# Optimization experiments

Hardware: AMD Instinct MI355X
Metric: run time of the kernel (lower is better)

The kernel has to match this reference:

```python
import jax, jax.numpy as jnp
import numpy as np

NUM_EMBEDDINGS = 16384
EMBEDDING_DIM = 256
B, C, H, W = 8, 256, 32, 32


def _l2_normalize(x, axis=-1, eps=1e-12):
    # matches torch.nn.functional.normalize(p=2): x / max(||x||, eps)
    n = jnp.sqrt(jnp.sum(x * x, axis=axis, keepdims=True))
    return x / jnp.maximum(n, eps)


def setup_inputs() -> dict:
    key = jax.random.key(0)
    k1, k2 = jax.random.split(key)
    z = jax.random.normal(k1, (B, C, H, W), dtype=jnp.float32)
    embedding_weight = jax.random.normal(k2, (NUM_EMBEDDINGS, EMBEDDING_DIM), dtype=jnp.float32)
    return {"z": z, "embedding_weight": embedding_weight}


def reference(z, embedding_weight):
    batch_size, channels, height, width = z.shape
    # [B,C,H,W] -> [B,H,W,C] -> [N, D]
    z_flat = jnp.transpose(z, (0, 2, 3, 1)).reshape(-1, EMBEDDING_DIM)
    z_flat = _l2_normalize(z_flat)                 # l2_norm=True
    emb = _l2_normalize(embedding_weight)
    # squared distances: ||z||^2 + ||e||^2 - 2 z e^T  -> [N, K]
    d = (jnp.sum(z_flat * z_flat, axis=1, keepdims=True)
         + jnp.sum(emb * emb, axis=1)
         - 2.0 * jnp.matmul(z_flat, emb.T))
    indices = jnp.argmin(d, axis=1)                # [N]
    z_q = emb[indices].reshape(batch_size, height, width, EMBEDDING_DIM)
    z_q = jnp.transpose(z_q, (0, 3, 1, 2))         # [B,C,H,W]
    indices = indices.reshape(batch_size, height, width)
    return z_q, indices
```

## Files before the change

### kernel.cpp

```cpp
#include <hip/hip_runtime.h>

#define NUM_E   16384
#define DIM     256
#define NROWS   8192
#define HW      1024
#define BM      128
#define BN      256
#define BK      32
#define NCB     (NUM_E / BN)
#define GATE    2e-3f
#define TAUC    2e-3f
#define EHID    2e-3
#define MAXC    16

#define SWZ(r) ((((r) >> 1) ^ ((r) >> 3)) & 3)

typedef __bf16 bf16x8 __attribute__((ext_vector_type(8)));
typedef float  f32x4  __attribute__((ext_vector_type(4)));
typedef float  f32x16 __attribute__((ext_vector_type(16)));

__device__ __forceinline__ unsigned short f2bf(float x) {
    unsigned u = __float_as_uint(x);
    unsigned r = (u + 0x7fffu + ((u >> 16) & 1u)) >> 16;
    return (unsigned short)r;
}
__device__ __forceinline__ void async_copy16(const void* g, void* l) {
    __builtin_amdgcn_global_load_lds(
        (const __attribute__((address_space(1))) unsigned int*)g,
        (__attribute__((address_space(3))) unsigned int*)l, 16, 0, 0);
}

__global__ void k_sumz(const float* __restrict__ z, float* __restrict__ zpart) {
    int n = blockIdx.x * 256 + threadIdx.x;
    int b = n >> 10, hw = n & 1023;
    int cb = blockIdx.y;
    const float* p = z + (size_t)(b * DIM + cb * 16) * HW + hw;
    float s = 0.f;
    #pragma unroll
    for (int c = 0; c < 16; c++) { float v = p[c * HW]; s += v * v; }
    zpart[cb * NROWS + n] = s;
}

__global__ void k_prep_z(const float* __restrict__ z, const float* __restrict__ zpart,
                         unsigned short* __restrict__ Zh) {
    __shared__ float T[64 * 68];
    __shared__ __align__(16) float Tinv[64];
    int t = threadIdx.x;
    int n0 = blockIdx.x * 64, c0 = blockIdx.y * 64;
    int b = n0 >> 10, hw0 = n0 & 1023;
    if (t < 64) {
        float s = 0.f;
        #pragma unroll
        for (int cb = 0; cb < 16; cb++) s += zpart[cb * NROWS + n0 + t];
        Tinv[t] = 1.0f / fmaxf(sqrtf(s), 1e-12f);
    }
    __syncthreads();
    #pragma unroll
    for (int i = 0; i < 4; i++) {
        int f = t + 256 * i;
        int cc = f >> 4, n4 = (f & 15) * 4;
        float4 v  = *(const float4*)(z + (size_t)(b * DIM + c0 + cc) * HW + hw0 + n4);
        float4 iv = *(const float4*)&Tinv[n4];
        v.x *= iv.x; v.y *= iv.y; v.z *= iv.z; v.w *= iv.w;
        *(float4*)&T[cc * 68 + n4] = v;
    }
    __syncthreads();
    #pragma unroll
    for (int i = 0; i < 4; i++) {
        int f = t + 256 * i;
        int nn = f >> 4, c4 = (f & 15) * 4;
        ushort4 h;
        h.x = f2bf(T[(c4+0)*68 + nn]);
        h.y = f2bf(T[(c4+1)*68 + nn]);
        h.z = f2bf(T[(c4+2)*68 + nn]);
        h.w = f2bf(T[(c4+3)*68 + nn]);
        *(ushort4*)(Zh + (size_t)(n0 + nn) * DIM + c0 + c4) = h;
    }
}

__global__ void k_prep_e(const float* __restrict__ emb, float* __restrict__ inv_e,
                         double* __restrict__ se2, unsigned short* __restrict__ Eh,
                         int* __restrict__ cnt, int* __restrict__ cnt2) {
    if (blockIdx.x == 0 && threadIdx.x == 0) { *cnt = 0; *cnt2 = 0; }
    int wv = threadIdx.x >> 6, lane = threadIdx.x & 63;
    int k = blockIdx.x * 4 + wv;
    float4 v = *(const float4*)(emb + (size_t)k * DIM + lane * 4);
    double sq = (double)v.x*v.x + (double)v.y*v.y + (double)v.z*v.z + (double)v.w*v.w;
    for (int off = 32; off > 0; off >>= 1) sq += __shfl_down(sq, off);
    double tot = fmax(__shfl(sq, 0), 1e-24);
    if (lane == 0) { se2[k] = tot; inv_e[k] = 1.0f / fmaxf((float)sqrt(tot), 1e-12f); }
    float s = 1.0f / fmaxf((float)sqrt(tot), 1e-12f);
    ushort4 h;
    h.x = f2bf(v.x * s); h.y = f2bf(v.y * s); h.z = f2bf(v.z * s); h.w = f2bf(v.w * s);
    *(ushort4*)(Eh + (size_t)k * DIM + lane * 4) = h;
}

__launch_bounds__(256, 2)
__global__ void k_score(const unsigned short* __restrict__ Zh,
                        const unsigned short* __restrict__ Eh, f32x4* __restrict__ part) {
    __shared__ __align__(16) float smem[16896];
    unsigned short* lds = (unsigned short*)smem;
    float* vals = smem;
    int*   idxs = (int*)(smem + 8448);
    const int t = threadIdx.x, l = t & 63, w = t >> 6;
    const int wm = w >> 1, wn = w & 1;
    const int m0 = blockIdx.x * BM;
    const int nb = blockIdx.y * BN;
    const int l31 = l & 31, lh = l >> 5;
    const int sr = l >> 2, sp = l & 3;

    const unsigned short* gA0 = Zh + (size_t)m0 * DIM;
    const unsigned short* gB0 = Eh + (size_t)nb * DIM;

    f32x16 acc[2][4];
    #pragma unroll
    for (int i = 0; i < 2; i++)
        #pragma unroll
        for (int j = 0; j < 4; j++) acc[i][j] = (f32x16)0.f;

    for (int kc = 0; kc < DIM; kc += BK) {
        {
            #pragma unroll
            for (int h = 0; h < 2; h++) {
                int sub = 4 * h + w;
                int r = sub * 16 + sr;
                int c = sp ^ SWZ(r);
                async_copy16(gA0 + (size_t)r * DIM + kc + c * 8, &lds[sub * 512]);
            }
        }
        #pragma unroll
        for (int h = 0; h < 4; h++) {
            int sub = 4 * h + w;
            int r = sub * 16 + sr;
            int c = sp ^ SWZ(r);
            async_copy16(gB0 + (size_t)r * DIM + kc + c * 8, &lds[4096 + sub * 512]);
        }
        __syncthreads();
        #pragma unroll
        for (int s = 0; s < 2; s++) {
            int c = 2 * s + lh;
            bf16x8 ah[2], bh[4];
            #pragma unroll
            for (int i = 0; i < 2; i++) {
                int r = wm * 64 + i * 32 + l31;
                ah[i] = *(const bf16x8*)&lds[r * 32 + ((c ^ SWZ(r)) * 8)];
            }
            #pragma unroll
            for (int j = 0; j < 4; j++) {
                int r = wn * 128 + j * 32 + l31;
                bh[j] = *(const bf16x8*)&lds[4096 + r * 32 + ((c ^ SWZ(r)) * 8)];
            }
            #pragma unroll
            for (int i = 0; i < 2; i++)
                #pragma unroll
                for (int j = 0; j < 4; j++)
                    acc[i][j] = __builtin_amdgcn_mfma_f32_32x32x16_bf16(ah[i], bh[j], acc[i][j], 0, 0, 0);
        }
        __syncthreads();
    }

    float VA1 = -2e9f, VA2 = -2e9f, VB1 = -2e9f, VB2 = -2e9f;
    int JA1 = 0, JA2 = 0, JB1 = 0, JB2 = 0;
    const int rl = t >> 2, q = t & 3;
    #pragma unroll
    for (int i = 0; i < 2; i++) {
        #pragma unroll
        for (int reg = 0; reg < 16; reg++) {
            float V1 = -2e9f, V2 = -2e9f; int I1 = 0, I2 = 0;
            #pragma unroll
            for (int j = 0; j < 4; j++) {
                float v = acc[i][j][reg];
                int c = nb + wn * 128 + j * 32 + l31;
                bool g1 = v > V1, g2 = v > V2;
                I2 = g1 ? I1 : (g2 ? c : I2);
                V2 = g1 ? V1 : (g2 ? v : V2);
                I1 = g1 ? c : I1;
                V1 = g1 ? v : V1;
            }
            int rr = wm * 32 + (reg & 3) + 8 * (reg >> 2) + 4 * lh;
            int s0 = wn * 64 + l31 * 2;
            int a0 = rr * 132 + (s0 >> 5) * 33 + (s0 & 31);
            vals[a0] = V1; vals[a0 + 1] = V2;
            idxs[a0] = I1; idxs[a0 + 1] = I2;
        }
        __syncthreads();
        float V1 = -2e9f, V2 = -2e9f; int I1 = 0, I2 = 0;
        const float* pv = &vals[rl * 132 + q * 33];
        const int*   pi = &idxs[rl * 132 + q * 33];
        #pragma unroll
        for (int u = 0; u < 32; u++) {
            float v = pv[u]; int c = pi[u];
            bool g1 = v > V1, g2 = v > V2;
            I2 = g1 ? I1 : (g2 ? c : I2);
            V2 = g1 ? V1 : (g2 ? v : V2);
            I1 = g1 ? c : I1;
            V1 = g1 ? v : V1;
        }
        __syncthreads();
        #pragma unroll
        for (int d = 1; d <= 2; d <<= 1) {
            float oV1 = __shfl_down(V1, d), oV2 = __shfl_down(V2, d);
            int   oI1 = __shfl_down(I1, d), oI2 = __shfl_down(I2, d);
            bool o1 = oV1 > V1;
            float mn = o1 ? V1 : oV1; int mni = o1 ? I1 : oI1;
            V1 = o1 ? oV1 : V1; I1 = o1 ? oI1 : I1;
            bool s2 = oV2 > V2;
            float m2 = s2 ? oV2 : V2; int m2i = s2 ? oI2 : I2;
            bool c2 = m2 > mn;
            V2 = c2 ? m2 : mn; I2 = c2 ? m2i : mni;
        }
        if (i == 0) {
            bool o1 = V1 > VA1;
            float mn = o1 ? VA1 : V1; int mni = o1 ? JA1 : I1;
            VA1 = o1 ? V1 : VA1; JA1 = o1 ? I1 : JA1;
            bool s2 = V2 > VA2;
            float m2 = s2 ? V2 : VA2; int m2i = s2 ? I2 : JA2;
            bool c2 = m2 > mn;
            VA2 = c2 ? m2 : mn; JA2 = c2 ? m2i : mni;
        } else {
            bool o1 = V1 > VB1;
            float mn = o1 ? VB1 : V1; int mni = o1 ? JB1 : I1;
            VB1 = o1 ? V1 : VB1; JB1 = o1 ? I1 : JB1;
            bool s2 = V2 > VB2;
            float m2 = s2 ? V2 : VB2; int m2i = s2 ? I2 : JB2;
            bool c2 = m2 > mn;
            VB2 = c2 ? m2 : mn; JB2 = c2 ? m2i : mni;
        }
    }
    if ((t & 3) == 0) {
        int rowA = (rl >> 5) * 64 + (rl & 31);
        int rowB = rowA + 32;
        f32x4 ea; ea[0] = VA1; ea[1] = __int_as_float(JA1);
        ea[2] = VA2; ea[3] = __int_as_float(JA2);
        part[(size_t)blockIdx.y * NROWS + m0 + rowA] = ea;
        f32x4 eb; eb[0] = VB1; eb[1] = __int_as_float(JB1);
        eb[2] = VB2; eb[3] = __int_as_float(JB2);
        part[(size_t)blockIdx.y * NROWS + m0 + rowB] = eb;
    }
}

__global__ void k_final(const f32x4* __restrict__ part, int* __restrict__ idx_ws,
                        float* __restrict__ out_idx, int* __restrict__ flags,
                        int* __restrict__ cnt, int* __restrict__ cand,
                        int* __restrict__ ccnt, float* __restrict__ v2q) {
    __shared__ f32x4 red[8][32];
    __shared__ float bcV1[32], bcV2[32];
    __shared__ int   lcc[32];
    __shared__ int   lcand[32][MAXC];
    __shared__ float sv2[8][32];
    const int nl = threadIdx.x & 31, sc = threadIdx.x >> 5;
    const int n = blockIdx.x * 32 + nl;
    if (threadIdx.x < 32) lcc[threadIdx.x] = 0;
    float V1 = -2e9f, V2 = -2e9f; int I1 = 0;
    for (int s = sc * 8; s < sc * 8 + 8; s++) {
        f32x4 e = part[(size_t)s * NROWS + n];
        float v1 = e[0]; int i1 = __float_as_int(e[1]); float v2 = e[2];
        V2 = fmaxf(fmaxf(V2, v2), fminf(v1, V1));
        I1 = (v1 > V1) ? i1 : I1;
        V1 = fmaxf(V1, v1);
    }
    f32x4 me; me[0] = V1; me[1] = __int_as_float(I1); me[2] = V2; me[3] = 0.f;
    red[sc][nl] = me;
    __syncthreads();
    if (threadIdx.x < 32) {
        float W1 = -2e9f, W2 = -2e9f; int J1 = 0;
        #pragma unroll
        for (int s2 = 0; s2 < 8; s2++) {
            f32x4 e = red[s2][threadIdx.x];
            float v1 = e[0]; int i1 = __float_as_int(e[1]); float v2 = e[2];
            W2 = fmaxf(fmaxf(W2, v2), fminf(v1, W1));
            J1 = (v1 > W1) ? i1 : J1;
            W1 = fmaxf(W1, v1);
        }
        int nn = blockIdx.x * 32 + threadIdx.x;
        idx_ws[nn] = J1;
        out_idx[nn] = (float)J1;
        bcV1[threadIdx.x] = W1;
        bcV2[threadIdx.x] = W2;
    }
    __syncthreads();
    float thr = bcV1[nl] - TAUC;
    float lv2 = -2e9f;
    for (int s = sc * 8; s < sc * 8 + 8; s++) {
        f32x4 e = part[(size_t)s * NROWS + n];
        if (e[0] >= thr) {
            int pos = atomicAdd(&lcc[nl], 2);
            if (pos < MAXC)     lcand[nl][pos]     = __float_as_int(e[1]);
            if (pos + 1 < MAXC) lcand[nl][pos + 1] = __float_as_int(e[3]);
            lv2 = fmaxf(lv2, e[2]);
        }
    }
    sv2[sc][nl] = lv2;
    __syncthreads();
    if (threadIdx.x < 32) {
        int nn = blockIdx.x * 32 + threadIdx.x;
        float W1 = bcV1[threadIdx.x], W2 = bcV2[threadIdx.x];
        if (W1 - W2 < GATE) {
            float m = -2e9f;
            #pragma unroll
            for (int s2 = 0; s2 < 8; s2++) m = fmaxf(m, sv2[s2][threadIdx.x]);
            int p = atomicAdd(cnt, 1);
            flags[p] = nn;
            ccnt[nn] = lcc[threadIdx.x];
            v2q[nn] = m;
            #pragma unroll
            for (int j = 0; j < MAXC; j++) cand[nn * MAXC + j] = lcand[threadIdx.x][j];
        }
    }
}

__launch_bounds__(256)
__global__ void k_rescan_cand(const int* __restrict__ flags, const int* __restrict__ cnt,
                              const int* __restrict__ cand, const int* __restrict__ ccnt,
                              const float* __restrict__ v2q,
                              const float* __restrict__ z, const float* __restrict__ emb,
                              const double* __restrict__ se2,
                              int* __restrict__ idx_ws, float* __restrict__ out_idx,
                              int* __restrict__ flags2, int* __restrict__ cnt2) {
    __shared__ double zs[DIM];
    __shared__ double wv[4];
    __shared__ int    wi[4];
    const int t = threadIdx.x, l = t & 63, w = t >> 6;
    const int F = *cnt;
    for (int f = blockIdx.x; f < F; f += gridDim.x) {
        int n = flags[f];
        int C = ccnt[n];
        int b = n >> 10, hw = n & 1023;
        __syncthreads();
        zs[t] = (double)z[(size_t)(b * DIM + t) * HW + hw];
        __syncthreads();
        double best = -2e18; int bi = 0x7fffffff;
        if (C <= MAXC) {
            double z0 = zs[l*4], z1 = zs[l*4+1], z2 = zs[l*4+2], z3 = zs[l*4+3];
            for (int cix = w; cix < C; cix += 4) {
                int k = cand[n * MAXC + cix];
                float4 ev = *(const float4*)(emb + (size_t)k * DIM + l * 4);
                double d = z0 * (double)ev.x + z1 * (double)ev.y
                         + z2 * (double)ev.z + z3 * (double)ev.w;
                #pragma unroll
                for (int o = 32; o > 0; o >>= 1) d += __shfl_down(d, o);
                if (l == 0) {
                    double qv = d / sqrt(se2[k]);
                    if (qv > best || (qv == best && k < bi)) { best = qv; bi = k; }
                }
            }
        }
        if (l == 0) { wv[w] = best; wi[w] = bi; }
        __syncthreads();
        if (t == 0) {
            if (C > MAXC) {
                int p = atomicAdd(cnt2, 1); flags2[p] = n;
            } else {
                double B = wv[0]; int BI = wi[0];
                #pragma unroll
                for (int x = 1; x < 4; x++)
                    if (wv[x] > B || (wv[x] == B && wi[x] < BI)) { B = wv[x]; BI = wi[x]; }
                if ((double)v2q[n] >= B - EHID) {
                    int p = atomicAdd(cnt2, 1); flags2[p] = n;
                } else {
                    idx_ws[n] = BI; out_idx[n] = (float)BI;
                }
            }
        }
    }
}

__launch_bounds__(256)
__global__ void k_fullscan_part(const int* __restrict__ flags2, const int* __restrict__ cnt2,
                                const float* __restrict__ z, const float* __restrict__ emb,
                                const double* __restrict__ se2, double2* __restrict__ partial) {
    __shared__ double zs[DIM];
    __shared__ double wv[4];
    __shared__ int    wi[4];
    const int t = threadIdx.x, l = t & 63, w = t >> 6;
    const int W = (*cnt2) * 64;
    for (int item = blockIdx.x; item < W; item += gridDim.x) {
        int f = item >> 6, split = item & 63;
        int n = flags2[f];
        int b = n >> 10, hw = n & 1023;
        __syncthreads();
        zs[t] = (double)z[(size_t)(b * DIM + t) * HW + hw];
        __syncthreads();
        double z0 = zs[l*4], z1 = zs[l*4+1], z2 = zs[l*4+2], z3 = zs[l*4+3];
        double best = -2e18; int bi = 0;
        int kbase = split * 256 + w * 64;
        for (int p = 0; p < 64; p++) {
            int k = kbase + p;
            float4 ev = *(const float4*)(emb + (size_t)k * DIM + l * 4);
            double d = z0 * (double)ev.x + z1 * (double)ev.y
                     + z2 * (double)ev.z + z3 * (double)ev.w;
            #pragma unroll
            for (int o = 32; o > 0; o >>= 1) d += __shfl_down(d, o);
            if (l == 0) {
                double qv = d / sqrt(se2[k]);
                if (qv > best) { best = qv; bi = k; }
            }
        }
        if (l == 0) { wv[w] = best; wi[w] = bi; }
        __syncthreads();
        if (t == 0) {
            double B = wv[0]; int BI = wi[0];
            #pragma unroll
            for (int x = 1; x < 4; x++)
                if (wv[x] > B || (wv[x] == B && wi[x] < BI)) { B = wv[x]; BI = wi[x]; }
            partial[item] = make_double2(B, (double)BI);
        }
        __syncthreads();
    }
}

__global__ void k_fullscan_merge(const int* __restrict__ flags2, const int* __restrict__ cnt2,
                                 const double2* __restrict__ partial,
                                 int* __restrict__ idx_ws, float* __restrict__ out_idx) {
    const int F = *cnt2;
    const int l = threadIdx.x & 63, w = threadIdx.x >> 6;
    for (int f = blockIdx.x * 4 + w; f < F; f += gridDim.x * 4) {
        double2 e = partial[(size_t)f * 64 + l];
        double v = e.x; int i = (int)e.y;
        #pragma unroll
        for (int o = 32; o > 0; o >>= 1) {
            double ov = __shfl_down(v, o);
            int    oi = __shfl_down(i, o);
            if (ov > v || (ov == v && oi < i)) { v = ov; i = oi; }
        }
        if (l == 0) { int n = flags2[f]; idx_ws[n] = i; out_idx[n] = (float)i; }
    }
}

__global__ void k_zq(const int* __restrict__ idx_ws, const float* __restrict__ emb,
                     const float* __restrict__ inv_e, float* __restrict__ zq) {
    int t = threadIdx.x;
    int n = blockIdx.x * 256 + t;
    int b = n >> 10, hw = n & 1023;
    int c0 = blockIdx.y * 32;
    int id = idx_ws[n];
    float s = inv_e[id];
    const float* er = emb + (size_t)id * DIM;
    #pragma unroll
    for (int cc = 0; cc < 32; cc += 4) {
        float4 a = *(const float4*)(er + c0 + cc);
        zq[(size_t)(b * DIM + c0 + cc + 0) * HW + hw] = a.x * s;
        zq[(size_t)(b * DIM + c0 + cc + 1) * HW + hw] = a.y * s;
        zq[(size_t)(b * DIM + c0 + cc + 2) * HW + hw] = a.z * s;
        zq[(size_t)(b * DIM + c0 + cc + 3) * HW + hw] = a.w * s;
    }
}

extern "C" void kernel_launch(void* const* d_in, const int* in_sizes, int n_in,
                              void* d_out, int out_size, void* d_ws, size_t ws_size,
                              hipStream_t stream) {
    const float* z   = (const float*)d_in[0];
    const float* emb = (const float*)d_in[1];

    unsigned short* Zh = (unsigned short*)d_ws;
    unsigned short* Eh = Zh + (size_t)NROWS * DIM;
    float*  inv_e = (float*)(Eh + (size_t)NUM_E * DIM);
    float*  zpart = inv_e + NUM_E;
    int*    idx_ws = (int*)(zpart + 16 * NROWS);
    double* se2   = (double*)(idx_ws + NROWS);
    int*    flags = (int*)(se2 + NUM_E);
    int*    flags2 = flags + NROWS;
    int*    cand  = flags2 + NROWS;
    int*    ccnt  = cand + NROWS * MAXC;
    float*  v2q   = (float*)(ccnt + NROWS);
    int*    cnt   = (int*)(v2q + NROWS);
    int*    cnt2  = cnt + 1;

    float* zq      = (float*)d_out;
    float* out_idx = zq + (size_t)NROWS * DIM;
    f32x4*   part    = (f32x4*)zq;
    double2* partial = (double2*)zq;

    k_sumz   <<<dim3(NROWS / 256, 16), 256, 0, stream>>>(z, zpart);
    k_prep_z <<<dim3(NROWS / 64, DIM / 64), 256, 0, stream>>>(z, zpart, Zh);
    k_prep_e <<<NUM_E / 4, 256, 0, stream>>>(emb, inv_e, se2, Eh, cnt, cnt2);
    k_score  <<<dim3(NROWS / BM, NCB), 256, 0, stream>>>(Zh, Eh, part);
    k_final  <<<NROWS / 32, 256, 0, stream>>>(part, idx_ws, out_idx, flags, cnt,
                                              cand, ccnt, v2q);
    k_rescan_cand  <<<1024, 256, 0, stream>>>(flags, cnt, cand, ccnt, v2q, z, emb,
                                              se2, idx_ws, out_idx, flags2, cnt2);
    k_fullscan_part<<<2048, 256, 0, stream>>>(flags2, cnt2, z, emb, se2, partial);
    k_fullscan_merge<<<64, 256, 0, stream>>>(flags2, cnt2, partial, idx_ws, out_idx);
    k_zq     <<<dim3(NROWS / 256, 8), 256, 0, stream>>>(idx_ws, emb, inv_e, zq);
}
```

Before: 204.7 us.

## Fuse z-norm into prep, shuffle-based score epilogue, merge candidate rescan into final

Folds the separate sum-of-squares kernel into k_prep_z, so each block loads a full 64-row by 256-channel tile, computes the norms in LDS and writes normalized bf16. The k_score epilogue now reduces top-2 across lanes with xor shuffles instead of an LDS scatter and re-scan, which shrinks shared memory enough to raise launch bounds to 3 blocks per SM. The candidate rescan is done inside k_final using shared-memory candidate lists, removing one launch and the global cand/ccnt/v2q buffers. The costs are a larger LDS tile in prep_z (about 70KB) with fewer blocks, and serial per-flag rescans within each final block.

```diff
diff --git a/kernel.cpp b/kernel.cpp
--- a/kernel.cpp
+++ b/kernel.cpp
@@ -30,58 +30,51 @@
         (__attribute__((address_space(3))) unsigned int*)l, 16, 0, 0);
 }
 
-__global__ void k_sumz(const float* __restrict__ z, float* __restrict__ zpart) {
-    int n = blockIdx.x * 256 + threadIdx.x;
-    int b = n >> 10, hw = n & 1023;
-    int cb = blockIdx.y;
-    const float* p = z + (size_t)(b * DIM + cb * 16) * HW + hw;
-    float s = 0.f;
+__global__ void k_prep_z(const float* __restrict__ z, unsigned short* __restrict__ Zh) {
+    __shared__ float T[256 * 68];
+    __shared__ float Tinv[64];
+    int t = threadIdx.x;
+    int n0 = blockIdx.x * 64;
+    int b = n0 >> 10, hw0 = n0 & 1023;
     #pragma unroll
-    for (int c = 0; c < 16; c++) { float v = p[c * HW]; s += v * v; }
-    zpart[cb * NROWS + n] = s;
-}
-
-__global__ void k_prep_z(const float* __restrict__ z, const float* __restrict__ zpart,
-                         unsigned short* __restrict__ Zh) {
-    __shared__ float T[64 * 68];
-    __shared__ __align__(16) float Tinv[64];
-    int t = threadIdx.x;
-    int n0 = blockIdx.x * 64, c0 = blockIdx.y * 64;
-    int b = n0 >> 10, hw0 = n0 & 1023;
-    if (t < 64) {
-        float s = 0.f;
-        #pragma unroll
-        for (int cb = 0; cb < 16; cb++) s += zpart[cb * NROWS + n0 + t];
-        Tinv[t] = 1.0f / fmaxf(sqrtf(s), 1e-12f);
-    }
-    __syncthreads();
-    #pragma unroll
-    for (int i = 0; i < 4; i++) {
+    for (int i = 0; i < 16; i++) {
         int f = t + 256 * i;
         int cc = f >> 4, n4 = (f & 15) * 4;
-        float4 v  = *(const float4*)(z + (size_t)(b * DIM + c0 + cc) * HW + hw0 + n4);
-        float4 iv = *(const float4*)&Tinv[n4];
-        v.x *= iv.x; v.y *= iv.y; v.z *= iv.z; v.w *= iv.w;
+        float4 v = *(const float4*)(z + (size_t)(b * DIM + cc) * HW + hw0 + n4);
         *(float4*)&T[cc * 68 + n4] = v;
     }
     __syncthreads();
+    {
+        int rl = t >> 2, q = t & 3;
+        float s = 0.f;
+        #pragma unroll
+        for (int c = q * 64; c < q * 64 + 64; c++) {
+            float v = T[c * 68 + rl];
+            s += v * v;
+        }
+        s += __shfl_down(s, 1);
+        s += __shfl_down(s, 2);
+        if (q == 0) Tinv[rl] = 1.0f / fmaxf(sqrtf(s), 1e-12f);
+    }
+    __syncthreads();
     #pragma unroll
-    for (int i = 0; i < 4; i++) {
+    for (int i = 0; i < 16; i++) {
         int f = t + 256 * i;
-        int nn = f >> 4, c4 = (f & 15) * 4;
+        int nn = f >> 6, c4 = (f & 63) * 4;
+        float iv = Tinv[nn];
         ushort4 h;
-        h.x = f2bf(T[(c4+0)*68 + nn]);
-        h.y = f2bf(T[(c4+1)*68 + nn]);
-        h.z = f2bf(T[(c4+2)*68 + nn]);
-        h.w = f2bf(T[(c4+3)*68 + nn]);
-        *(ushort4*)(Zh + (size_t)(n0 + nn) * DIM + c0 + c4) = h;
+        h.x = f2bf(T[(c4+0)*68 + nn] * iv);
+        h.y = f2bf(T[(c4+1)*68 + nn] * iv);
+        h.z = f2bf(T[(c4+2)*68 + nn] * iv);
+        h.w = f2bf(T[(c4+3)*68 + nn] * iv);
+        *(ushort4*)(Zh + (size_t)(n0 + nn) * DIM + c4) = h;
     }
 }
 
 __global__ void k_prep_e(const float* __restrict__ emb, float* __restrict__ inv_e,
                          double* __restrict__ se2, unsigned short* __restrict__ Eh,
-                         int* __restrict__ cnt, int* __restrict__ cnt2) {
-    if (blockIdx.x == 0 && threadIdx.x == 0) { *cnt = 0; *cnt2 = 0; }
+                         int* __restrict__ cnt2) {
+    if (blockIdx.x == 0 && threadIdx.x == 0) *cnt2 = 0;
     int wv = threadIdx.x >> 6, lane = threadIdx.x & 63;
     int k = blockIdx.x * 4 + wv;
     float4 v = *(const float4*)(emb + (size_t)k * DIM + lane * 4);
@@ -95,13 +88,10 @@
     *(ushort4*)(Eh + (size_t)k * DIM + lane * 4) = h;
 }
 
-__launch_bounds__(256, 2)
+__launch_bounds__(256, 3)
 __global__ void k_score(const unsigned short* __restrict__ Zh,
                         const unsigned short* __restrict__ Eh, f32x4* __restrict__ part) {
-    __shared__ __align__(16) float smem[16896];
-    unsigned short* lds = (unsigned short*)smem;
-    float* vals = smem;
-    int*   idxs = (int*)(smem + 8448);
+    __shared__ __align__(16) unsigned short lds[12288];
     const int t = threadIdx.x, l = t & 63, w = t >> 6;
     const int wm = w >> 1, wn = w & 1;
     const int m0 = blockIdx.x * BM;
@@ -119,14 +109,12 @@
         for (int j = 0; j < 4; j++) acc[i][j] = (f32x16)0.f;
 
     for (int kc = 0; kc < DIM; kc += BK) {
-        {
-            #pragma unroll
-            for (int h = 0; h < 2; h++) {
-                int sub = 4 * h + w;
-                int r = sub * 16 + sr;
-                int c = sp ^ SWZ(r);
-                async_copy16(gA0 + (size_t)r * DIM + kc + c * 8, &lds[sub * 512]);
-            }
+        #pragma unroll
+        for (int h = 0; h < 2; h++) {
+            int sub = 4 * h + w;
+            int r = sub * 16 + sr;
+            int c = sp ^ SWZ(r);
+            async_copy16(gA0 + (size_t)r * DIM + kc + c * 8, &lds[sub * 512]);
         }
         #pragma unroll
         for (int h = 0; h < 4; h++) {
@@ -159,9 +147,7 @@
         __syncthreads();
     }
 
-    float VA1 = -2e9f, VA2 = -2e9f, VB1 = -2e9f, VB2 = -2e9f;
-    int JA1 = 0, JA2 = 0, JB1 = 0, JB2 = 0;
-    const int rl = t >> 2, q = t & 3;
+    f32x4* mrg = (f32x4*)lds;
     #pragma unroll
     for (int i = 0; i < 2; i++) {
         #pragma unroll
@@ -177,80 +163,66 @@
                 I1 = g1 ? c : I1;
                 V1 = g1 ? v : V1;
             }
-            int rr = wm * 32 + (reg & 3) + 8 * (reg >> 2) + 4 * lh;
-            int s0 = wn * 64 + l31 * 2;
-            int a0 = rr * 132 + (s0 >> 5) * 33 + (s0 & 31);
-            vals[a0] = V1; vals[a0 + 1] = V2;
-            idxs[a0] = I1; idxs[a0 + 1] = I2;
-        }
-        __syncthreads();
-        float V1 = -2e9f, V2 = -2e9f; int I1 = 0, I2 = 0;
-        const float* pv = &vals[rl * 132 + q * 33];
-        const int*   pi = &idxs[rl * 132 + q * 33];
-        #pragma unroll
-        for (int u = 0; u < 32; u++) {
-            float v = pv[u]; int c = pi[u];
-            bool g1 = v > V1, g2 = v > V2;
-            I2 = g1 ? I1 : (g2 ? c : I2);
-            V2 = g1 ? V1 : (g2 ? v : V2);
-            I1 = g1 ? c : I1;
-            V1 = g1 ? v : V1;
-        }
-        __syncthreads();
-        #pragma unroll
-        for (int d = 1; d <= 2; d <<= 1) {
-            float oV1 = __shfl_down(V1, d), oV2 = __shfl_down(V2, d);
-            int   oI1 = __shfl_down(I1, d), oI2 = __shfl_down(I2, d);
-            bool o1 = oV1 > V1;
-            float mn = o1 ? V1 : oV1; int mni = o1 ? I1 : oI1;
-            V1 = o1 ? oV1 : V1; I1 = o1 ? oI1 : I1;
-            bool s2 = oV2 > V2;
-            float m2 = s2 ? oV2 : V2; int m2i = s2 ? oI2 : I2;
-            bool c2 = m2 > mn;
-            V2 = c2 ? m2 : mn; I2 = c2 ? m2i : mni;
-        }
-        if (i == 0) {
-            bool o1 = V1 > VA1;
-            float mn = o1 ? VA1 : V1; int mni = o1 ? JA1 : I1;
-            VA1 = o1 ? V1 : VA1; JA1 = o1 ? I1 : JA1;
-            bool s2 = V2 > VA2;
-            float m2 = s2 ? V2 : VA2; int m2i = s2 ? I2 : JA2;
-            bool c2 = m2 > mn;
-            VA2 = c2 ? m2 : mn; JA2 = c2 ? m2i : mni;
-        } else {
-            bool o1 = V1 > VB1;
-            float mn = o1 ? VB1 : V1; int mni = o1 ? JB1 : I1;
-            VB1 = o1 ? V1 : VB1; JB1 = o1 ? I1 : JB1;
-            bool s2 = V2 > VB2;
-            float m2 = s2 ? V2 : VB2; int m2i = s2 ? I2 : JB2;
-            bool c2 = m2 > mn;
-            VB2 = c2 ? m2 : mn; JB2 = c2 ? m2i : mni;
-        }
-    }
-    if ((t & 3) == 0) {
-        int rowA = (rl >> 5) * 64 + (rl & 31);
-        int rowB = rowA + 32;
-        f32x4 ea; ea[0] = VA1; ea[1] = __int_as_float(JA1);
-        ea[2] = VA2; ea[3] = __int_as_float(JA2);
-        part[(size_t)blockIdx.y * NROWS + m0 + rowA] = ea;
-        f32x4 eb; eb[0] = VB1; eb[1] = __int_as_float(JB1);
-        eb[2] = VB2; eb[3] = __int_as_float(JB2);
-        part[(size_t)blockIdx.y * NROWS + m0 + rowB] = eb;
-    }
-}
-
-__global__ void k_final(const f32x4* __restrict__ part, int* __restrict__ idx_ws,
-                        float* __restrict__ out_idx, int* __restrict__ flags,
-                        int* __restrict__ cnt, int* __restrict__ cand,
-                        int* __restrict__ ccnt, float* __restrict__ v2q) {
+            #pragma unroll
+            for (int m = 1; m <= 16; m <<= 1) {
+                float oV1 = __shfl_xor(V1, m), oV2 = __shfl_xor(V2, m);
+                int   oI1 = __shfl_xor(I1, m), oI2 = __shfl_xor(I2, m);
+                bool o1 = oV1 > V1;
+                float mn = o1 ? V1 : oV1; int mni = o1 ? I1 : oI1;
+                V1 = o1 ? oV1 : V1; I1 = o1 ? oI1 : I1;
+                bool s2 = oV2 > V2;
+                float m2 = s2 ? oV2 : V2; int m2i = s2 ? oI2 : I2;
+                bool c2 = m2 > mn;
+                V2 = c2 ? m2 : mn; I2 = c2 ? m2i : mni;
+            }
+            if (l31 == 0) {
+                int row = wm * 64 + i * 32 + (reg & 3) + 8 * (reg >> 2) + 4 * lh;
+                f32x4 e; e[0] = V1; e[1] = __int_as_float(I1);
+                e[2] = V2; e[3] = __int_as_float(I2);
+                mrg[row * 2 + wn] = e;
+            }
+        }
+    }
+    __syncthreads();
+    if (t < BM) {
+        f32x4 a = mrg[t * 2], bq = mrg[t * 2 + 1];
+        float V1 = a[0], V2 = a[2]; int I1 = __float_as_int(a[1]), I2 = __float_as_int(a[3]);
+        float oV1 = bq[0], oV2 = bq[2];
+        int   oI1 = __float_as_int(bq[1]), oI2 = __float_as_int(bq[3]);
+        bool o1 = oV1 > V1;
+        float mn = o1 ? V1 : oV1; int mni = o1 ? I1 : oI1;
+        V1 = o1 ? oV1 : V1; I1 = o1 ? oI1 : I1;
+        bool s2 = oV2 > V2;
+        float m2 = s2 ? oV2 : V2; int m2i = s2 ? oI2 : I2;
+        bool c2 = m2 > mn;
+        V2 = c2 ? m2 : mn; I2 = c2 ? m2i : mni;
+        f32x4 e; e[0] = V1; e[1] = __int_as_float(I1);
+        e[2] = V2; e[3] = __int_as_float(I2);
+        part[(size_t)blockIdx.y * NROWS + m0 + t] = e;
+    }
+}
+
+__global__ void k_final(const f32x4* __restrict__ part,
+                        const float* __restrict__ z, const float* __restrict__ emb,
+                        const double* __restrict__ se2,
+                        int* __restrict__ idx_ws, float* __restrict__ out_idx,
+                        int* __restrict__ flags2, int* __restrict__ cnt2) {
     __shared__ f32x4 red[8][32];
-    __shared__ float bcV1[32], bcV2[32];
+    __shared__ float bcV1[32];
     __shared__ int   lcc[32];
     __shared__ int   lcand[32][MAXC];
     __shared__ float sv2[8][32];
-    const int nl = threadIdx.x & 31, sc = threadIdx.x >> 5;
+    __shared__ float mv2[32];
+    __shared__ int   fl[32];
+    __shared__ int   nf;
+    __shared__ double zs[DIM];
+    __shared__ double wvv[4];
+    __shared__ int    wii[4];
+    const int t = threadIdx.x;
+    const int nl = t & 31, sc = t >> 5;
     const int n = blockIdx.x * 32 + nl;
-    if (threadIdx.x < 32) lcc[threadIdx.x] = 0;
+    if (t < 32) lcc[t] = 0;
+    if (t == 0) nf = 0;
     float V1 = -2e9f, V2 = -2e9f; int I1 = 0;
     for (int s = sc * 8; s < sc * 8 + 8; s++) {
         f32x4 e = part[(size_t)s * NROWS + n];
@@ -262,21 +234,21 @@
     f32x4 me; me[0] = V1; me[1] = __int_as_float(I1); me[2] = V2; me[3] = 0.f;
     red[sc][nl] = me;
     __syncthreads();
-    if (threadIdx.x < 32) {
-        float W1 = -2e9f, W2 = -2e9f; int J1 = 0;
+    float W1 = -2e9f, W2 = -2e9f;
+    if (t < 32) {
+        int J1 = 0;
         #pragma unroll
         for (int s2 = 0; s2 < 8; s2++) {
-            f32x4 e = red[s2][threadIdx.x];
+            f32x4 e = red[s2][t];
             float v1 = e[0]; int i1 = __float_as_int(e[1]); float v2 = e[2];
             W2 = fmaxf(fmaxf(W2, v2), fminf(v1, W1));
             J1 = (v1 > W1) ? i1 : J1;
             W1 = fmaxf(W1, v1);
         }
-        int nn = blockIdx.x * 32 + threadIdx.x;
+        int nn = blockIdx.x * 32 + t;
         idx_ws[nn] = J1;
         out_idx[nn] = (float)J1;
-        bcV1[threadIdx.x] = W1;
-        bcV2[threadIdx.x] = W2;
+        bcV1[t] = W1;
     }
     __syncthreads();
     float thr = bcV1[nl] - TAUC;
@@ -292,48 +264,31 @@
     }
     sv2[sc][nl] = lv2;
     __syncthreads();
-    if (threadIdx.x < 32) {
-        int nn = blockIdx.x * 32 + threadIdx.x;
-        float W1 = bcV1[threadIdx.x], W2 = bcV2[threadIdx.x];
+    if (t < 32) {
         if (W1 - W2 < GATE) {
             float m = -2e9f;
             #pragma unroll
-            for (int s2 = 0; s2 < 8; s2++) m = fmaxf(m, sv2[s2][threadIdx.x]);
-            int p = atomicAdd(cnt, 1);
-            flags[p] = nn;
-            ccnt[nn] = lcc[threadIdx.x];
-            v2q[nn] = m;
-            #pragma unroll
-            for (int j = 0; j < MAXC; j++) cand[nn * MAXC + j] = lcand[threadIdx.x][j];
-        }
-    }
-}
-
-__launch_bounds__(256)
-__global__ void k_rescan_cand(const int* __restrict__ flags, const int* __restrict__ cnt,
-                              const int* __restrict__ cand, const int* __restrict__ ccnt,
-                              const float* __restrict__ v2q,
-                              const float* __restrict__ z, const float* __restrict__ emb,
-                              const double* __restrict__ se2,
-                              int* __restrict__ idx_ws, float* __restrict__ out_idx,
-                              int* __restrict__ flags2, int* __restrict__ cnt2) {
-    __shared__ double zs[DIM];
-    __shared__ double wv[4];
-    __shared__ int    wi[4];
-    const int t = threadIdx.x, l = t & 63, w = t >> 6;
-    const int F = *cnt;
-    for (int f = blockIdx.x; f < F; f += gridDim.x) {
-        int n = flags[f];
-        int C = ccnt[n];
-        int b = n >> 10, hw = n & 1023;
-        __syncthreads();
+            for (int s2 = 0; s2 < 8; s2++) m = fmaxf(m, sv2[s2][t]);
+            mv2[t] = m;
+            int p = atomicAdd(&nf, 1);
+            fl[p] = t;
+        }
+    }
+    __syncthreads();
+    const int NF = nf;
+    const int l = t & 63, w = t >> 6;
+    for (int fi = 0; fi < NF; fi++) {
+        int nl2 = fl[fi];
+        int C = lcc[nl2];
+        int n2 = blockIdx.x * 32 + nl2;
+        int b = n2 >> 10, hw = n2 & 1023;
         zs[t] = (double)z[(size_t)(b * DIM + t) * HW + hw];
         __syncthreads();
         double best = -2e18; int bi = 0x7fffffff;
         if (C <= MAXC) {
             double z0 = zs[l*4], z1 = zs[l*4+1], z2 = zs[l*4+2], z3 = zs[l*4+3];
             for (int cix = w; cix < C; cix += 4) {
-                int k = cand[n * MAXC + cix];
+                int k = lcand[nl2][cix];
                 float4 ev = *(const float4*)(emb + (size_t)k * DIM + l * 4);
                 double d = z0 * (double)ev.x + z1 * (double)ev.y
                          + z2 * (double)ev.z + z3 * (double)ev.w;
@@ -345,23 +300,24 @@
                 }
             }
         }
-        if (l == 0) { wv[w] = best; wi[w] = bi; }
+        if (l == 0) { wvv[w] = best; wii[w] = bi; }
         __syncthreads();
         if (t == 0) {
             if (C > MAXC) {
-                int p = atomicAdd(cnt2, 1); flags2[p] = n;
+                flags2[atomicAdd(cnt2, 1)] = n2;
             } else {
-                double B = wv[0]; int BI = wi[0];
+                double B = wvv[0]; int BI = wii[0];
                 #pragma unroll
                 for (int x = 1; x < 4; x++)
-                    if (wv[x] > B || (wv[x] == B && wi[x] < BI)) { B = wv[x]; BI = wi[x]; }
-                if ((double)v2q[n] >= B - EHID) {
-                    int p = atomicAdd(cnt2, 1); flags2[p] = n;
+                    if (wvv[x] > B || (wvv[x] == B && wii[x] < BI)) { B = wvv[x]; BI = wii[x]; }
+                if ((double)mv2[nl2] >= B - EHID) {
+                    flags2[atomicAdd(cnt2, 1)] = n2;
                 } else {
-                    idx_ws[n] = BI; out_idx[n] = (float)BI;
+                    idx_ws[n2] = BI; out_idx[n2] = (float)BI;
                 }
             }
         }
+        __syncthreads();
     }
 }
 
@@ -455,30 +411,21 @@
     unsigned short* Zh = (unsigned short*)d_ws;
     unsigned short* Eh = Zh + (size_t)NROWS * DIM;
     float*  inv_e = (float*)(Eh + (size_t)NUM_E * DIM);
-    float*  zpart = inv_e + NUM_E;
-    int*    idx_ws = (int*)(zpart + 16 * NROWS);
+    int*    idx_ws = (int*)(inv_e + NUM_E);
     double* se2   = (double*)(idx_ws + NROWS);
-    int*    flags = (int*)(se2 + NUM_E);
-    int*    flags2 = flags + NROWS;
-    int*    cand  = flags2 + NROWS;
-    int*    ccnt  = cand + NROWS * MAXC;
-    float*  v2q   = (float*)(ccnt + NROWS);
-    int*    cnt   = (int*)(v2q + NROWS);
-    int*    cnt2  = cnt + 1;
+    int*    flags2 = (int*)(se2 + NUM_E);
+    int*    cnt2  = flags2 + NROWS;
 
     float* zq      = (float*)d_out;
     float* out_idx = zq + (size_t)NROWS * DIM;
     f32x4*   part    = (f32x4*)zq;
     double2* partial = (double2*)zq;
 
-    k_sumz   <<<dim3(NROWS / 256, 16), 256, 0, stream>>>(z, zpart);
-    k_prep_z <<<dim3(NROWS / 64, DIM / 64), 256, 0, stream>>>(z, zpart, Zh);
-    k_prep_e <<<NUM_E / 4, 256, 0, stream>>>(emb, inv_e, se2, Eh, cnt, cnt2);
+    k_prep_z <<<NROWS / 64, 256, 0, stream>>>(z, Zh);
+    k_prep_e <<<NUM_E / 4, 256, 0, stream>>>(emb, inv_e, se2, Eh, cnt2);
     k_score  <<<dim3(NROWS / BM, NCB), 256, 0, stream>>>(Zh, Eh, part);
-    k_final  <<<NROWS / 32, 256, 0, stream>>>(part, idx_ws, out_idx, flags, cnt,
-                                              cand, ccnt, v2q);
-    k_rescan_cand  <<<1024, 256, 0, stream>>>(flags, cnt, cand, ccnt, v2q, z, emb,
-                                              se2, idx_ws, out_idx, flags2, cnt2);
+    k_final  <<<NROWS / 32, 256, 0, stream>>>(part, z, emb, se2, idx_ws, out_idx,
+                                              flags2, cnt2);
     k_fullscan_part<<<2048, 256, 0, stream>>>(flags2, cnt2, z, emb, se2, partial);
     k_fullscan_merge<<<64, 256, 0, stream>>>(flags2, cnt2, partial, idx_ws, out_idx);
     k_zq     <<<dim3(NROWS / 256, 8), 256, 0, stream>>>(idx_ws, emb, inv_e, zq);
```

New measurement: 286.6 us. 1.4x slower.
